# Optimization experiments

Measured on AMD Instinct MI355X. Metric: run time of the kernel, lower is better.

Reference implementation:

```python
import jax, jax.numpy as jnp
import numpy as np

RADIUS = 2
TEMP = 1.0
B, CIN, D, H, W = 1, 32, 64, 64, 64
PROJ, OUT = 64, 64
K = (2 * RADIUS + 1) ** 3  # 125 local offsets

_OFFSETS = np.array([(dz, dy, dx)
                     for dz in range(-RADIUS, RADIUS + 1)
                     for dy in range(-RADIUS, RADIUS + 1)
                     for dx in range(-RADIUS, RADIUS + 1)], dtype=np.int32)


def _conv3d(x, w, b, pad):
    y = jax.lax.conv_general_dilated(
        x, w, window_strides=(1, 1, 1), padding=[(pad, pad)] * 3,
        dimension_numbers=('NCDHW', 'OIDHW', 'NCDHW'))
    if b is not None:
        y = y + b[None, :, None, None, None]
    return y


def _l2norm(x):
    # torch F.normalize(dim=1): x / max(||x||_2, 1e-12)
    n = jnp.sqrt(jnp.sum(x * x, axis=1, keepdims=True))
    return x / jnp.maximum(n, 1e-12)


def _inorm(x, eps=1e-5):
    # InstanceNorm3d (affine=False): normalize over spatial dims per (B,C)
    mu = jnp.mean(x, axis=(2, 3, 4), keepdims=True)
    var = jnp.mean((x - mu) ** 2, axis=(2, 3, 4), keepdims=True)
    return (x - mu) * jax.lax.rsqrt(var + eps)


def _ntn(x):
    return jnp.nan_to_num(x, nan=0.0, posinf=0.0, neginf=0.0)


def setup_inputs() -> dict:
    key = jax.random.key(0)
    ks = jax.random.split(key, 8)
    s = 0.05
    return {
        'source_features': jax.random.normal(ks[0], (B, CIN, D, H, W), jnp.float32),
        'warped_target_features': jax.random.normal(ks[1], (B, CIN, D, H, W), jnp.float32),
        'w_src': jax.random.normal(ks[2], (PROJ, CIN, 1, 1, 1), jnp.float32) * s,
        'b_src': jnp.zeros((PROJ,), jnp.float32),
        'w_tgt': jax.random.normal(ks[3], (PROJ, CIN, 1, 1, 1), jnp.float32) * s,
        'b_tgt': jnp.zeros((PROJ,), jnp.float32),
        'w_enc1': jax.random.normal(ks[4], (OUT, K + 5, 3, 3, 3), jnp.float32) * s,
        'b_enc1': jnp.zeros((OUT,), jnp.float32),
        'w_enc2': jax.random.normal(ks[5], (OUT, OUT, 3, 3, 3), jnp.float32) * s,
        'b_enc2': jnp.zeros((OUT,), jnp.float32),
    }


def reference(source_features, warped_target_features, w_src, b_src, w_tgt, b_tgt,
              w_enc1, b_enc1, w_enc2, b_enc2):
    sp = _l2norm(_conv3d(source_features, w_src, b_src, 0))      # [B,P,D,H,W]
    tp = _l2norm(_conv3d(warped_target_features, w_tgt, b_tgt, 0))
    pt = jnp.pad(tp, ((0, 0), (0, 0), (RADIUS, RADIUS), (RADIUS, RADIUS), (RADIUS, RADIUS)),
                 mode='edge')  # replicate pad

    starts = jnp.asarray(_OFFSETS + RADIUS, jnp.int32)  # [K,3] slice starts

    def corr_one(st):
        sh = jax.lax.dynamic_slice(pt, (0, 0, st[0], st[1], st[2]), (B, PROJ, D, H, W))
        return jnp.sum(sp * sh, axis=1)  # [B,D,H,W]

    corr = jnp.transpose(jax.vmap(corr_one)(starts), (1, 0, 2, 3, 4))  # [B,K,D,H,W]
    scaled = corr / max(TEMP, 1e-6)

    top2 = jax.lax.top_k(jnp.moveaxis(scaled, 1, -1), 2)[0]  # [B,D,H,W,2]
    m = jnp.moveaxis(top2[..., 0:1], -1, 1)   # running max   [B,1,D,H,W]
    s2 = jnp.moveaxis(top2[..., 1:2], -1, 1)  # second max

    p = jnp.exp(scaled - m)                    # [B,K,D,H,W]
    Z = jnp.sum(p, axis=1, keepdims=True)
    inv = 1.0 / jnp.maximum(Z, 1e-8)

    offv = jnp.asarray(_OFFSETS, jnp.float32)  # [K,3]
    expected_offset = _ntn(jnp.einsum('bkdhw,kc->bcdhw', p, offv) * inv)
    confidence = _ntn(jnp.minimum(inv, 1.0))   # max-prob = exp(m-m)/Z
    second_prob = jnp.exp(s2 - m) * inv
    margin = _ntn(jnp.maximum(confidence - second_prob, 0.0))
    entropy = _ntn(m + jnp.log(jnp.maximum(Z, 1e-8))
                   - jnp.sum(p * scaled, axis=1, keepdims=True) * inv)

    enc_in = jnp.concatenate([corr, expected_offset, confidence, entropy], axis=1)  # [B,K+5,D,H,W]
    h = _conv3d(enc_in, w_enc1, b_enc1, 1)
    h = jax.nn.gelu(_inorm(h), approximate=False)
    h = _conv3d(h, w_enc2, b_enc2, 1)
    h = jax.nn.gelu(_inorm(h), approximate=False)
    encoded_features = _ntn(h)

    return expected_offset, confidence, margin, entropy, encoded_features
```

## Files before the change

kernel.cpp:

```cpp
#include <hip/hip_runtime.h>

#define DEV __device__ __forceinline__

typedef short bf16x8 __attribute__((ext_vector_type(8)));
typedef float f32x4 __attribute__((ext_vector_type(4)));

static const int NVOX = 262144;

DEV float bflo(unsigned int u) { return __uint_as_float(u << 16); }
DEV float bfhi(unsigned int u) { return __uint_as_float(u & 0xffff0000u); }
DEV float bf2f(unsigned short s) { return __uint_as_float(((unsigned int)s) << 16); }
DEV unsigned short f2bf(float f) {
    unsigned int x = __float_as_uint(f);
    x += 0x7fffu + ((x >> 16) & 1u);
    return (unsigned short)(x >> 16);
}
DEV float ldin(const void* p, int i, int f) {
    return f ? ((const float*)p)[i] : bf2f(((const unsigned short*)p)[i]);
}

DEV void gld16(const unsigned short* g, unsigned short* l) {
    __builtin_amdgcn_global_load_lds(
        (const __attribute__((address_space(1))) unsigned int*)g,
        (__attribute__((address_space(3))) unsigned int*)l, 16, 0, 0);
}

__global__ void sniff_kernel(const unsigned short* __restrict__ src, int* __restrict__ flag) {
    __shared__ int cnt[256];
    int t = threadIdx.x;
    int c = 0;
    for (int i = t; i < 4096; i += 256) {
        unsigned int u = (unsigned int)src[i] & 0x7fffu;
        c += (u >= 0x4900u) ? 1 : 0;
    }
    cnt[t] = c;
    __syncthreads();
    for (int s = 128; s > 0; s >>= 1) {
        if (t < s) cnt[t] += cnt[t + s];
        __syncthreads();
    }
    if (t == 0) *flag = (cnt[0] > 8) ? 1 : 0;
}

__global__ void prep_kernel(const void* __restrict__ w1, const void* __restrict__ w2,
                            const void* __restrict__ bsv, const void* __restrict__ btv,
                            const void* __restrict__ b1v, const void* __restrict__ b2v,
                            const int* __restrict__ flag,
                            unsigned short* __restrict__ Wf1,
                            unsigned short* __restrict__ Wf2,
                            float* __restrict__ fbias) {
    const int f = *flag;
    int idx = blockIdx.x * 256 + threadIdx.x;
    const int N1  = 27 * 4 * 4 * 512;
    const int N1E = 2 * 4 * 512;
    const int N2  = 27 * 2 * 4 * 512;
    if (idx < N1) {
        int frag = idx >> 9;
        int r    = idx & 511;
        int lane = r >> 3, j = r & 7;
        int nt = frag & 3;
        int tk = frag >> 2;
        int tap = tk >> 2, kc = tk & 3;
        int o  = nt * 16 + (lane & 15);
        int cp = kc * 32 + (lane >> 4) * 8 + j;
        Wf1[idx] = f2bf(ldin(w1, (o * 130 + cp) * 27 + tap, f));
    } else if (idx < N1 + N1E) {
        int i2 = idx - N1;
        int frag = i2 >> 9;
        int r    = i2 & 511;
        int lane = r >> 3, j = r & 7;
        int nt = frag & 3, kc = frag >> 2;
        int o   = nt * 16 + (lane & 15);
        int kap = kc * 32 + (lane >> 4) * 8 + j;
        unsigned short val = 0;
        if (kap < 54) {
            int tap = kap >> 1, ch = 128 + (kap & 1);
            val = f2bf(ldin(w1, (o * 130 + ch) * 27 + tap, f));
        }
        Wf1[idx] = val;
    } else if (idx < N1 + N1E + N2) {
        int i2 = idx - N1 - N1E;
        int frag = i2 >> 9;
        int r    = i2 & 511;
        int lane = r >> 3, j = r & 7;
        int nt = frag & 3;
        int tk = frag >> 2;
        int tap = tk >> 1, kc = tk & 1;
        int o = nt * 16 + (lane & 15);
        int c = kc * 32 + (lane >> 4) * 8 + j;
        Wf2[i2] = f2bf(ldin(w2, (o * 64 + c) * 27 + tap, f));
    } else if (idx < N1 + N1E + N2 + 256) {
        int j = idx - N1 - N1E - N2;
        const void* bp = (j < 64) ? bsv : (j < 128) ? btv : (j < 192) ? b1v : b2v;
        fbias[j] = ldin(bp, j & 63, f);
    }
}

__global__ __launch_bounds__(256) void proj_kernel(
        const void* __restrict__ Xsrc, const void* __restrict__ Xtgt,
        const void* __restrict__ Wsrc, const void* __restrict__ Wtgt,
        const float* __restrict__ fbias, const int* __restrict__ flag,
        unsigned short* __restrict__ SP, unsigned short* __restrict__ TP) {
    const int f = *flag;
    const void* Xin = blockIdx.y ? Xtgt : Xsrc;
    const void* W   = blockIdx.y ? Wtgt : Wsrc;
    const float* Bb = fbias + (blockIdx.y ? 64 : 0);
    unsigned short* Outp = blockIdx.y ? TP : SP;

    __shared__ float ws[2048];
    const int t = threadIdx.x;
    for (int i = t; i < 2048; i += 256) {
        int ci = i >> 6, o = i & 63;
        ws[i] = ldin(W, o * 32 + ci, f);
    }
    __syncthreads();

    const size_t v = (size_t)blockIdx.x * 256 + t;
    float acc[64];
#pragma unroll
    for (int o = 0; o < 64; ++o) acc[o] = Bb[o];
    if (f) {
        const float* Xf = (const float*)Xin;
        for (int ci = 0; ci < 32; ++ci) {
            float x = Xf[(size_t)ci * NVOX + v];
            const float4* wr = (const float4*)(ws + ci * 64);
#pragma unroll
            for (int o4 = 0; o4 < 16; ++o4) {
                float4 w4 = wr[o4];
                acc[o4 * 4 + 0] = fmaf(w4.x, x, acc[o4 * 4 + 0]);
                acc[o4 * 4 + 1] = fmaf(w4.y, x, acc[o4 * 4 + 1]);
                acc[o4 * 4 + 2] = fmaf(w4.z, x, acc[o4 * 4 + 2]);
                acc[o4 * 4 + 3] = fmaf(w4.w, x, acc[o4 * 4 + 3]);
            }
        }
    } else {
        const unsigned short* Xb = (const unsigned short*)Xin;
        for (int ci = 0; ci < 32; ++ci) {
            float x = bf2f(Xb[(size_t)ci * NVOX + v]);
            const float4* wr = (const float4*)(ws + ci * 64);
#pragma unroll
            for (int o4 = 0; o4 < 16; ++o4) {
                float4 w4 = wr[o4];
                acc[o4 * 4 + 0] = fmaf(w4.x, x, acc[o4 * 4 + 0]);
                acc[o4 * 4 + 1] = fmaf(w4.y, x, acc[o4 * 4 + 1]);
                acc[o4 * 4 + 2] = fmaf(w4.z, x, acc[o4 * 4 + 2]);
                acc[o4 * 4 + 3] = fmaf(w4.w, x, acc[o4 * 4 + 3]);
            }
        }
    }
    float s = 0.f;
#pragma unroll
    for (int o = 0; o < 64; ++o) s = fmaf(acc[o], acc[o], s);
    float scale = 1.f / fmaxf(sqrtf(s), 1e-12f);

    unsigned int pk[32];
#pragma unroll
    for (int o = 0; o < 32; ++o)
        pk[o] = (unsigned int)f2bf(acc[2 * o] * scale) |
                ((unsigned int)f2bf(acc[2 * o + 1] * scale) << 16);
    uint4* outp = (uint4*)(Outp + v * 64);
#pragma unroll
    for (int j = 0; j < 8; ++j)
        outp[j] = make_uint4(pk[4 * j], pk[4 * j + 1], pk[4 * j + 2], pk[4 * j + 3]);
}

__global__ __launch_bounds__(256) void corr_kernel(
        const unsigned short* __restrict__ SP, const unsigned short* __restrict__ TP,
        unsigned short* __restrict__ X1, float* __restrict__ Out) {
    __shared__ __align__(16) unsigned short tpb[2][80 * 64];
    __shared__ __align__(16) unsigned short sband[2][64 * 128];

    const int t = threadIdx.x;
    const int wv = t >> 6, lane = t & 63;
    const int q = lane >> 4, l16 = lane & 15;
    const int x0 = wv * 16;

    const int bid = blockIdx.x;
    const int wg = (bid & 7) * 256 + (bid >> 3);
    const int z = wg >> 5, y = (wg & 31) * 2;
    const size_t vb0 = ((size_t)z * 64 + y) * 64;
    const size_t vb1 = vb0 + 64;

    const unsigned short* ar0 = SP + (vb0 + x0 + l16) * 64 + q * 8;
    const unsigned short* ar1 = SP + (vb1 + x0 + l16) * 64 + q * 8;
    const bf16x8 a00 = *(const bf16x8*)(ar0);
    const bf16x8 a01 = *(const bf16x8*)(ar0 + 32);
    const bf16x8 a10 = *(const bf16x8*)(ar1);
    const bf16x8 a11 = *(const bf16x8*)(ar1 + 32);

    auto stage_tp = [&](int it, int b) {
        const int zc = min(max(z + it / 6 - 2, 0), 63);
        const int yc = min(max(y - 2 + it % 6, 0), 63);
        const unsigned short* tb = TP + ((size_t)zc * 64 + yc) * 4096;
#pragma unroll
        for (int j = 0; j < 2; ++j) {
            int c = t + j * 256;
            int pp = c >> 3, cc = c & 7;
            int xc = min(max(pp - 2, 0), 63);
            gld16(tb + xc * 64 + ((cc ^ (pp & 7)) * 8),
                  &tpb[b][(wv * 64 + j * 256) * 8]);
        }
        if (wv < 2) {
            int c = 512 + wv * 64 + lane;
            int pp = c >> 3, cc = c & 7;
            int xc = min(max(pp - 2, 0), 63);
            gld16(tb + xc * 64 + ((cc ^ (pp & 7)) * 8),
                  &tpb[b][(512 + wv * 64) * 8]);
        }
    };

    stage_tp(0, 0);
    __syncthreads();

    int p = 0;
    for (int it = 0; it < 30; ++it) {
        if (it < 29) stage_tp(it + 1, p ^ 1);
        const int dz = it / 6, j = it % 6;
        const bool r0 = (j < 5), r1 = (j > 0);

        f32x4 acc0[2] = {{0.f, 0.f, 0.f, 0.f}, {0.f, 0.f, 0.f, 0.f}};
        f32x4 acc1[2] = {{0.f, 0.f, 0.f, 0.f}, {0.f, 0.f, 0.f, 0.f}};
        {
            const char* tb = (const char*)tpb[p];
#pragma unroll
            for (int nt = 0; nt < 2; ++nt) {
                const int pr = x0 + nt * 16 + l16;
                bf16x8 b0 = *(const bf16x8*)(tb + pr * 128 + ((q ^ (pr & 7)) * 16));
                bf16x8 b1 = *(const bf16x8*)(tb + pr * 128 + (((4 + q) ^ (pr & 7)) * 16));
                if (r0) {
                    acc0[nt] = __builtin_amdgcn_mfma_f32_16x16x32_bf16(a00, b0, acc0[nt], 0, 0, 0);
                    acc0[nt] = __builtin_amdgcn_mfma_f32_16x16x32_bf16(a01, b1, acc0[nt], 0, 0, 0);
                }
                if (r1) {
                    acc1[nt] = __builtin_amdgcn_mfma_f32_16x16x32_bf16(a10, b0, acc1[nt], 0, 0, 0);
                    acc1[nt] = __builtin_amdgcn_mfma_f32_16x16x32_bf16(a11, b1, acc1[nt], 0, 0, 0);
                }
            }
        }
        if (r0) {
            const int kb = dz * 25 + j * 5;
            char* sg = (char*)sband[0];
#pragma unroll
            for (int nt = 0; nt < 2; ++nt)
#pragma unroll
                for (int r = 0; r < 4; ++r) {
                    int ml = q * 4 + r;
                    int dxp = nt * 16 + l16 - ml;
                    if ((unsigned)dxp < 5u) {
                        int xl = x0 + ml;
                        *(unsigned short*)(sg + xl * 256 + (((kb + dxp) * 2) ^ ((xl & 7) << 4))) =
                            f2bf(acc0[nt][r]);
                    }
                }
        }
        if (r1) {
            const int kb = dz * 25 + (j - 1) * 5;
            char* sg = (char*)sband[1];
#pragma unroll
            for (int nt = 0; nt < 2; ++nt)
#pragma unroll
                for (int r = 0; r < 4; ++r) {
                    int ml = q * 4 + r;
                    int dxp = nt * 16 + l16 - ml;
                    if ((unsigned)dxp < 5u) {
                        int xl = x0 + ml;
                        *(unsigned short*)(sg + xl * 256 + (((kb + dxp) * 2) ^ ((xl & 7) << 4))) =
                            f2bf(acc1[nt][r]);
                    }
                }
        }
        __syncthreads();
        p ^= 1;
    }

    for (int half = 0; half < 2; ++half) {
        const size_t vbase = half ? vb1 : vb0;
        const int vox = t >> 2, part = t & 3;
        const int sx = (vox & 7) << 4;
        const char* sg = (const char*)sband[half];
        uint4 u[4];
#pragma unroll
        for (int j = 0; j < 4; ++j)
            u[j] = *(const uint4*)(sg + vox * 256 + ((part * 64 + j * 16) ^ sx));

        float m = -1e30f, s2 = -1e30f;
#pragma unroll
        for (int j = 0; j < 4; ++j) {
            const unsigned int uu[4] = {u[j].x, u[j].y, u[j].z, u[j].w};
#pragma unroll
            for (int w = 0; w < 4; ++w) {
                int k = part * 32 + j * 8 + w * 2;
                float d0 = (k < 125) ? bflo(uu[w]) : -1e30f;
                float d1 = (k + 1 < 125) ? bfhi(uu[w]) : -1e30f;
                float lo0 = fminf(d0, m); m = fmaxf(d0, m); s2 = fmaxf(s2, lo0);
                float lo1 = fminf(d1, m); m = fmaxf(d1, m); s2 = fmaxf(s2, lo1);
            }
        }
#pragma unroll
        for (int off = 1; off <= 2; off <<= 1) {
            float om = __shfl_xor(m, off, 64);
            float os = __shfl_xor(s2, off, 64);
            float lo = fminf(m, om);
            m = fmaxf(m, om);
            s2 = fmaxf(fmaxf(s2, os), lo);
        }
        int kk = part * 32;
        int dz0 = kk / 25, rem = kk - dz0 * 25, dy0 = rem / 5, dx0 = rem - dy0 * 5;
        float fx = (float)(dx0 - 2), fy = (float)(dy0 - 2), fz = (float)(dz0 - 2);
        float Zs = 0.f, S1 = 0.f, Ox = 0.f, Oy = 0.f, Oz = 0.f;
#pragma unroll
        for (int j = 0; j < 4; ++j) {
            const unsigned int uu[4] = {u[j].x, u[j].y, u[j].z, u[j].w};
#pragma unroll
            for (int w = 0; w < 8; ++w) {
                int k = part * 32 + j * 8 + w;
                bool ok = (k < 125);
                float d = (w & 1) ? bfhi(uu[w >> 1]) : bflo(uu[w >> 1]);
                d = ok ? d : 0.f;
                float e = ok ? __expf(d - m) : 0.f;
                Zs += e; S1 = fmaf(e, d, S1);
                Ox = fmaf(e, fx, Ox); Oy = fmaf(e, fy, Oy); Oz = fmaf(e, fz, Oz);
                fx += 1.f;
                if (fx > 2.5f) { fx = -2.f; fy += 1.f; if (fy > 2.5f) { fy = -2.f; fz += 1.f; } }
            }
        }
#pragma unroll
        for (int off = 1; off <= 2; off <<= 1) {
            Zs += __shfl_xor(Zs, off, 64);
            S1 += __shfl_xor(S1, off, 64);
            Ox += __shfl_xor(Ox, off, 64);
            Oy += __shfl_xor(Oy, off, 64);
            Oz += __shfl_xor(Oz, off, 64);
        }
        if (part == 0) {
            float inv  = 1.f / fmaxf(Zs, 1e-8f);
            float eoz = Oz * inv, eoy = Oy * inv, eox = Ox * inv;
            float conf = fminf(inv, 1.f);
            float marg = fmaxf(conf - __expf(s2 - m) * inv, 0.f);
            float ent  = m + __logf(fmaxf(Zs, 1e-8f)) - S1 * inv;
            char* sgw = (char*)sband[half];
            *(unsigned short*)(sgw + vox * 256 + (250 ^ sx)) = f2bf(eoz);
            *(unsigned short*)(sgw + vox * 256 + (252 ^ sx)) = f2bf(eoy);
            *(unsigned short*)(sgw + vox * 256 + (254 ^ sx)) = f2bf(eox);
            const size_t v = vbase + vox;
            *(unsigned int*)(X1 + v * 160 + 128) =
                (unsigned int)f2bf(conf) | ((unsigned int)f2bf(ent) << 16);
            Out[v]                    = eoz;
            Out[(size_t)NVOX + v]     = eoy;
            Out[(size_t)2 * NVOX + v] = eox;
            Out[(size_t)3 * NVOX + v] = conf;
            Out[(size_t)4 * NVOX + v] = marg;
            Out[(size_t)5 * NVOX + v] = ent;
        }
    }
    __syncthreads();

#pragma unroll
    for (int j = 0; j < 8; ++j) {
        int i = t + j * 256;
        int row = i >> 10, rr = i & 1023;
        int vox = rr >> 4, cc = rr & 15;
        *(uint4*)(X1 + ((row ? vb1 : vb0) + vox) * 160 + (size_t)cc * 8) =
            *(const uint4*)((const char*)sband[row] + vox * 256 + ((cc * 16) ^ ((vox & 7) << 4)));
    }
}

template <int XSTRIDE, int CPAD, int KC, int NLD, int MINW, bool TAIL>
__global__ __launch_bounds__(256, MINW) void conv3_kernel(
        const unsigned short* __restrict__ Xin, const unsigned short* __restrict__ Wf,
        const unsigned short* __restrict__ Wfe,
        const float* __restrict__ Bias, unsigned short* __restrict__ Out) {
    constexpr int SLOT = 66 * CPAD;
    constexpr int CH16 = CPAD / 8;
    __shared__ __align__(16) unsigned short lds[3 * SLOT];
    const int lin = blockIdx.x;
    const int wg = (lin & 7) * 256 + (lin >> 3);
    const int z = wg >> 5;
    const int y = (wg & 31) * 2;
    const int t = threadIdx.x;
    const int wv = t >> 6, lane = t & 63;
    const int quad = lane >> 4, l16 = lane & 15;
    const int ml2 = (wv & 1) * 2;
    const int nt2 = (wv >> 1) * 2;

    f32x4 acc[2][2][2] = {};

    auto stage_plane = [&](int pidx) {
        const int zz = z + (pidx >> 2) - 1;
        const int py = y + (pidx & 3) - 1;
        if ((unsigned)zz >= 64u || (unsigned)py >= 64u) return;
        const unsigned short* base = Xin + (((size_t)zz * 64 + py) * 64) * XSTRIDE;
        unsigned short* dst = lds + (pidx % 3) * SLOT + CPAD;
#pragma unroll
        for (int i = 0; i < NLD; ++i) {
            int chunk = wv * 64 + lane + i * 256;
            int xi = chunk / CH16;
            int cc = chunk % CH16;
            gld16(base + xi * XSTRIDE + ((cc ^ ((xi + 1) & 7)) * 8),
                  dst + (size_t)(wv * 64 + i * 256) * 8);
        }
    };

    if (TAIL) {
        unsigned short* ebuf = lds;
#pragma unroll
        for (int i2 = 0; i2 < 16; ++i2) {
            int i = t + i2 * 256;
            int vox = i >> 5, slot = i & 31;
            unsigned int val = 0u;
            int kap;
            if (slot < 27) {
                int ddz = slot / 9 - 1, ddy = (slot / 3) % 3 - 1, dxx = slot % 3 - 1;
                int zz = z + ddz, yy = y + (vox >> 6) + ddy, xx = (vox & 63) + dxx;
                kap = slot * 2;
                if ((unsigned)zz < 64u && (unsigned)yy < 64u && (unsigned)xx < 64u)
                    val = *(const unsigned int*)(Xin + (((size_t)zz * 64 + yy) * 64 + xx) * XSTRIDE + 128);
            } else {
                kap = 54 + (slot - 27) * 2;
            }
            *(unsigned int*)(ebuf + (size_t)vox * 72 + kap) = val;
        }
        __syncthreads();
#pragma unroll
        for (int kc = 0; kc < 2; ++kc) {
            bf16x8 bte[2];
#pragma unroll
            for (int nl = 0; nl < 2; ++nl)
                bte[nl] = *(const bf16x8*)(Wfe + (size_t)(kc * 4 + nt2 + nl) * 512 + lane * 8);
#pragma unroll
            for (int r = 0; r < 2; ++r)
#pragma unroll
            for (int ml = 0; ml < 2; ++ml) {
                bf16x8 a = *(const bf16x8*)(ebuf + (size_t)(r * 64 + (ml2 + ml) * 16 + l16) * 72 + (kc * 4 + quad) * 8);
#pragma unroll
                for (int nl = 0; nl < 2; ++nl)
                    acc[r][ml][nl] = __builtin_amdgcn_mfma_f32_16x16x32_bf16(a, bte[nl], acc[r][ml][nl], 0, 0, 0);
            }
        }
        __syncthreads();
    }

    if (t < 6 * CH16) {
        int sl = t / (2 * CH16), r2 = (t / CH16) & 1, c = t % CH16;
        *(uint4*)(&lds[(size_t)sl * SLOT + (size_t)(r2 * 65) * CPAD + c * 8]) =
            make_uint4(0u, 0u, 0u, 0u);
    }
    stage_plane(0);
    stage_plane(1);
    __syncthreads();

    for (int i = 0; i < 9; ++i) {
        const int s0 = (i / 3) * 4 + i % 3;
        if (i == 3 || i == 6) {
            stage_plane(s0 + 1);
            __syncthreads();
        }
        if (s0 + 2 < 12) stage_plane(s0 + 2);

        const int zz = z + i / 3 - 1;
        const int dy = i % 3 - 1;
        const bool zok = (unsigned)zz < 64u;
        const bool rok0 = zok && (unsigned)(y + dy) < 64u;
        const bool rok1 = zok && (unsigned)(y + 1 + dy) < 64u;
        const unsigned short* sb0 = lds + (size_t)(s0 % 3) * SLOT;
        const unsigned short* sb1 = lds + (size_t)((s0 + 1) % 3) * SLOT;
        if (rok0 || rok1) {
#pragma unroll
            for (int dx = 0; dx < 3; ++dx) {
                const int tap = (i / 3) * 9 + (i % 3) * 3 + dx;
                const unsigned short* wt = Wf + ((size_t)tap * KC * 4) * 512 + lane * 8;
                bf16x8 bf[KC][2];
#pragma unroll
                for (int kc = 0; kc < KC; ++kc)
#pragma unroll
                    for (int nl = 0; nl < 2; ++nl)
                        bf[kc][nl] = *(const bf16x8*)(wt + (size_t)(kc * 4 + nt2 + nl) * 512);
#pragma unroll
                for (int kc = 0; kc < KC; ++kc) {
#pragma unroll
                    for (int ml = 0; ml < 2; ++ml) {
                        const int row = (ml2 + ml) * 16 + l16 + dx;
                        const int co = ((kc * 4 + quad) ^ (row & 7)) * 8;
                        if (rok0) {
                            bf16x8 a = *(const bf16x8*)(&sb0[(size_t)row * CPAD + co]);
#pragma unroll
                            for (int nl = 0; nl < 2; ++nl)
                                acc[0][ml][nl] = __builtin_amdgcn_mfma_f32_16x16x32_bf16(a, bf[kc][nl], acc[0][ml][nl], 0, 0, 0);
                        }
                        if (rok1) {
                            bf16x8 a = *(const bf16x8*)(&sb1[(size_t)row * CPAD + co]);
#pragma unroll
                            for (int nl = 0; nl < 2; ++nl)
                                acc[1][ml][nl] = __builtin_amdgcn_mfma_f32_16x16x32_bf16(a, bf[kc][nl], acc[1][ml][nl], 0, 0, 0);
                        }
                    }
                }
            }
        }
        __syncthreads();
    }

#pragma unroll
    for (int r = 0; r < 2; ++r) {
        const size_t vb = ((size_t)z * 64 + (y + r)) * 64;
#pragma unroll
        for (int ml = 0; ml < 2; ++ml) {
#pragma unroll
            for (int nl = 0; nl < 2; ++nl) {
                const int oc = (nt2 + nl) * 16 + l16;
                const float bv = Bias[oc];
#pragma unroll
                for (int rr = 0; rr < 4; ++rr)
                    Out[(vb + (ml2 + ml) * 16 + quad * 4 + rr) * 64 + oc] =
                        f2bf(acc[r][ml][nl][rr] + bv);
            }
        }
    }
}

__global__ __launch_bounds__(256) void stats_kernel(
        const unsigned short* __restrict__ H, float* __restrict__ stats) {
    const int t = threadIdx.x;
    const int c = t & 63, g = t >> 6;
    float s = 0.f, q = 0.f;
    for (int v = blockIdx.x * 4 + g; v < NVOX; v += gridDim.x * 4) {
        float x = bf2f(H[(size_t)v * 64 + c]);
        s += x; q = fmaf(x, x, q);
    }
    __shared__ float ls[256], lq[256];
    ls[t] = s; lq[t] = q;
    __syncthreads();
    if (t < 64) {
        s = ls[t] + ls[t + 64] + ls[t + 128] + ls[t + 192];
        q = lq[t] + lq[t + 64] + lq[t + 128] + lq[t + 192];
        atomicAdd(&stats[c], s);
        atomicAdd(&stats[64 + c], q);
    }
}

__global__ void finalize_kernel(const float* __restrict__ stats, float* __restrict__ musr) {
    int c = threadIdx.x;
    if (c < 64) {
        float mu  = stats[c] * (1.0f / 262144.0f);
        float var = stats[64 + c] * (1.0f / 262144.0f) - mu * mu;
        musr[c] = mu;
        musr[64 + c] = rsqrtf(var + 1e-5f);
    }
}

__global__ __launch_bounds__(256) void norm_gelu_kernel(
        const unsigned short* __restrict__ H, const float* __restrict__ musr,
        unsigned short* __restrict__ G) {
    const size_t base = ((size_t)blockIdx.x * 256 + threadIdx.x) * 8;
    uint4 u = *(const uint4*)(H + base);
    const int c0 = (int)(base & 63);
    const unsigned int uu[4] = {u.x, u.y, u.z, u.w};
    unsigned int w[4];
#pragma unroll
    for (int p = 0; p < 4; ++p) {
        int c = c0 + p * 2;
        float x0 = (bflo(uu[p]) - musr[c]) * musr[64 + c];
        float x1 = (bfhi(uu[p]) - musr[c + 1]) * musr[64 + c + 1];
        float g0 = 0.5f * x0 * (1.f + erff(x0 * 0.70710678118f));
        float g1 = 0.5f * x1 * (1.f + erff(x1 * 0.70710678118f));
        w[p] = (unsigned int)f2bf(g0) | ((unsigned int)f2bf(g1) << 16);
    }
    *(uint4*)(G + base) = make_uint4(w[0], w[1], w[2], w[3]);
}

__global__ __launch_bounds__(256) void out_final_kernel(
        const unsigned short* __restrict__ H2, const float* __restrict__ musr,
        float* __restrict__ OutEnc) {
    __shared__ float tile[64 * 260];
    const int t = threadIdx.x;
    const size_t v0 = (size_t)blockIdx.x * 256;
#pragma unroll
    for (int i = 0; i < 8; ++i) {
        int chunk = t + i * 256;
        uint4 u = *(const uint4*)(H2 + v0 * 64 + (size_t)chunk * 8);
        int vox = chunk >> 3;
        int c0 = (chunk & 7) * 8;
        const unsigned int uu[4] = {u.x, u.y, u.z, u.w};
#pragma unroll
        for (int p = 0; p < 4; ++p) {
            int c = c0 + p * 2;
            float x0 = (bflo(uu[p]) - musr[c]) * musr[64 + c];
            float x1 = (bfhi(uu[p]) - musr[c + 1]) * musr[64 + c + 1];
            tile[c * 260 + vox]       = 0.5f * x0 * (1.f + erff(x0 * 0.70710678118f));
            tile[(c + 1) * 260 + vox] = 0.5f * x1 * (1.f + erff(x1 * 0.70710678118f));
        }
    }
    __syncthreads();
    const int c = t >> 2, sub = t & 3;
#pragma unroll
    for (int iter = 0; iter < 16; ++iter) {
        int fq = iter * 4 + sub;
        float4 val = *(const float4*)(&tile[c * 260 + fq * 4]);
        *(float4*)(OutEnc + (size_t)c * NVOX + v0 + fq * 4) = val;
    }
}

extern "C" void kernel_launch(void* const* d_in, const int* in_sizes, int n_in,
                              void* d_out, int out_size, void* d_ws, size_t ws_size,
                              hipStream_t stream) {
    const void* src  = d_in[0];
    const void* tgt  = d_in[1];
    const void* wsrc = d_in[2];
    const void* bsrc = d_in[3];
    const void* wtgt = d_in[4];
    const void* btgt = d_in[5];
    const void* w1   = d_in[6];
    const void* b1   = d_in[7];
    const void* w2   = d_in[8];
    const void* b2   = d_in[9];
    float* out = (float*)d_out;

    char* ws = (char*)d_ws;
    unsigned short* TPb = (unsigned short*)(ws);
    unsigned short* SPb = (unsigned short*)(ws + 33554432);
    unsigned short* X1  = (unsigned short*)(ws + 67108864);
    unsigned short* Wf1 = (unsigned short*)(ws + 150994944);
    unsigned short* Wf2 = (unsigned short*)(ws + 151547904);
    int*   flag   = (int*)  (ws + 151769088);
    float* fbias  = (float*)(ws + 151769152);
    float* stats1 = (float*)(ws + 151770176);
    float* musr1  = (float*)(ws + 151770688);
    float* stats2 = (float*)(ws + 151771200);
    float* musr2  = (float*)(ws + 151771712);
    unsigned short* H1 = SPb;
    unsigned short* G1 = TPb;
    unsigned short* H2 = X1;
    unsigned short* Wf1e = Wf1 + 27 * 4 * 4 * 512;

    (void)hipMemsetAsync(stats1, 0, 2048, stream);
    sniff_kernel<<<1, 256, 0, stream>>>((const unsigned short*)src, flag);
    prep_kernel<<<1313, 256, 0, stream>>>(w1, w2, bsrc, btgt, b1, b2, flag, Wf1, Wf2, fbias);
    proj_kernel<<<dim3(1024, 2), 256, 0, stream>>>(src, tgt, wsrc, wtgt, fbias, flag, SPb, TPb);
    corr_kernel<<<2048, 256, 0, stream>>>(SPb, TPb, X1, out);
    conv3_kernel<160, 128, 4, 4, 3, true><<<2048, 256, 0, stream>>>(X1, Wf1, Wf1e, fbias + 128, H1);
    stats_kernel<<<256, 256, 0, stream>>>(H1, stats1);
    finalize_kernel<<<1, 64, 0, stream>>>(stats1, musr1);
    norm_gelu_kernel<<<8192, 256, 0, stream>>>(H1, musr1, G1);
    conv3_kernel<64, 64, 2, 2, 4, false><<<2048, 256, 0, stream>>>(G1, Wf2, nullptr, fbias + 192, H2);
    stats_kernel<<<256, 256, 0, stream>>>(H2, stats2);
    finalize_kernel<<<1, 64, 0, stream>>>(stats2, musr2);
    out_final_kernel<<<1024, 256, 0, stream>>>(H2, musr2, out + 6 * (size_t)NVOX);
}
```

Baseline: 695.2 us.

## Switch conv3 kernels to 32x32x16 MFMA with per-wave row ownership

Replaces the 16x16x32 bf16 MFMA tiling in both 3x3x3 conv kernels with 32x32x16 MFMA. Each wave now owns one output row and a 32-channel half of the outputs, and the weight fragment packing in prep_kernel is changed to match. The goal is fewer MFMA issues, fewer B-fragment loads per wave, and less branching on row validity. The cost is different LDS read patterns under the existing swizzle and a larger per-lane accumulator, which could add bank conflicts or register pressure.

```diff
diff --git a/kernel.cpp b/kernel.cpp
--- a/kernel.cpp
+++ b/kernel.cpp
@@ -4,6 +4,7 @@
 
 typedef short bf16x8 __attribute__((ext_vector_type(8)));
 typedef float f32x4 __attribute__((ext_vector_type(4)));
+typedef float f32x16 __attribute__((ext_vector_type(16)));
 
 static const int NVOX = 262144;
 
@@ -51,27 +52,27 @@
                             float* __restrict__ fbias) {
     const int f = *flag;
     int idx = blockIdx.x * 256 + threadIdx.x;
-    const int N1  = 27 * 4 * 4 * 512;
-    const int N1E = 2 * 4 * 512;
-    const int N2  = 27 * 2 * 4 * 512;
+    const int N1  = 27 * 8 * 2 * 512;
+    const int N1E = 4 * 2 * 512;
+    const int N2  = 27 * 4 * 2 * 512;
     if (idx < N1) {
         int frag = idx >> 9;
         int r    = idx & 511;
         int lane = r >> 3, j = r & 7;
-        int nt = frag & 3;
-        int tk = frag >> 2;
-        int tap = tk >> 2, kc = tk & 3;
-        int o  = nt * 16 + (lane & 15);
-        int cp = kc * 32 + (lane >> 4) * 8 + j;
+        int nt = frag & 1;
+        int tk = frag >> 1;
+        int tap = tk >> 3, kc = tk & 7;
+        int o  = nt * 32 + (lane & 31);
+        int cp = kc * 16 + (lane >> 5) * 8 + j;
         Wf1[idx] = f2bf(ldin(w1, (o * 130 + cp) * 27 + tap, f));
     } else if (idx < N1 + N1E) {
         int i2 = idx - N1;
         int frag = i2 >> 9;
         int r    = i2 & 511;
         int lane = r >> 3, j = r & 7;
-        int nt = frag & 3, kc = frag >> 2;
-        int o   = nt * 16 + (lane & 15);
-        int kap = kc * 32 + (lane >> 4) * 8 + j;
+        int nt = frag & 1, kc = frag >> 1;
+        int o   = nt * 32 + (lane & 31);
+        int kap = kc * 16 + (lane >> 5) * 8 + j;
         unsigned short val = 0;
         if (kap < 54) {
             int tap = kap >> 1, ch = 128 + (kap & 1);
@@ -83,11 +84,11 @@
         int frag = i2 >> 9;
         int r    = i2 & 511;
         int lane = r >> 3, j = r & 7;
-        int nt = frag & 3;
-        int tk = frag >> 2;
-        int tap = tk >> 1, kc = tk & 1;
-        int o = nt * 16 + (lane & 15);
-        int c = kc * 32 + (lane >> 4) * 8 + j;
+        int nt = frag & 1;
+        int tk = frag >> 1;
+        int tap = tk >> 2, kc = tk & 3;
+        int o = nt * 32 + (lane & 31);
+        int c = kc * 16 + (lane >> 5) * 8 + j;
         Wf2[i2] = f2bf(ldin(w2, (o * 64 + c) * 27 + tap, f));
     } else if (idx < N1 + N1E + N2 + 256) {
         int j = idx - N1 - N1E - N2;
@@ -379,11 +380,11 @@
     const int y = (wg & 31) * 2;
     const int t = threadIdx.x;
     const int wv = t >> 6, lane = t & 63;
-    const int quad = lane >> 4, l16 = lane & 15;
-    const int ml2 = (wv & 1) * 2;
-    const int nt2 = (wv >> 1) * 2;
-
-    f32x4 acc[2][2][2] = {};
+    const int ry = wv & 1;
+    const int nt = wv >> 1;
+    const int l31 = lane & 31, kh = lane >> 5;
+
+    f32x16 acc[2] = {};
 
     auto stage_plane = [&](int pidx) {
         const int zz = z + (pidx >> 2) - 1;
@@ -422,19 +423,13 @@
         }
         __syncthreads();
 #pragma unroll
-        for (int kc = 0; kc < 2; ++kc) {
-            bf16x8 bte[2];
-#pragma unroll
-            for (int nl = 0; nl < 2; ++nl)
-                bte[nl] = *(const bf16x8*)(Wfe + (size_t)(kc * 4 + nt2 + nl) * 512 + lane * 8);
-#pragma unroll
-            for (int r = 0; r < 2; ++r)
-#pragma unroll
-            for (int ml = 0; ml < 2; ++ml) {
-                bf16x8 a = *(const bf16x8*)(ebuf + (size_t)(r * 64 + (ml2 + ml) * 16 + l16) * 72 + (kc * 4 + quad) * 8);
-#pragma unroll
-                for (int nl = 0; nl < 2; ++nl)
-                    acc[r][ml][nl] = __builtin_amdgcn_mfma_f32_16x16x32_bf16(a, bte[nl], acc[r][ml][nl], 0, 0, 0);
+        for (int kc = 0; kc < 4; ++kc) {
+            bf16x8 bte = *(const bf16x8*)(Wfe + (size_t)(kc * 2 + nt) * 512 + lane * 8);
+#pragma unroll
+            for (int half = 0; half < 2; ++half) {
+                bf16x8 a = *(const bf16x8*)(ebuf +
+                    (size_t)((ry * 2 + half) * 32 + l31) * 72 + kc * 16 + kh * 8);
+                acc[half] = __builtin_amdgcn_mfma_f32_32x32x16_bf16(a, bte, acc[half], 0, 0, 0);
             }
         }
         __syncthreads();
@@ -459,40 +454,26 @@
 
         const int zz = z + i / 3 - 1;
         const int dy = i % 3 - 1;
-        const bool zok = (unsigned)zz < 64u;
-        const bool rok0 = zok && (unsigned)(y + dy) < 64u;
-        const bool rok1 = zok && (unsigned)(y + 1 + dy) < 64u;
-        const unsigned short* sb0 = lds + (size_t)(s0 % 3) * SLOT;
-        const unsigned short* sb1 = lds + (size_t)((s0 + 1) % 3) * SLOT;
-        if (rok0 || rok1) {
+        const bool ok = (unsigned)zz < 64u && (unsigned)(y + ry + dy) < 64u;
+        const unsigned short* sb = lds + (size_t)((s0 + ry) % 3) * SLOT;
+        if (ok) {
 #pragma unroll
             for (int dx = 0; dx < 3; ++dx) {
                 const int tap = (i / 3) * 9 + (i % 3) * 3 + dx;
-                const unsigned short* wt = Wf + ((size_t)tap * KC * 4) * 512 + lane * 8;
-                bf16x8 bf[KC][2];
+                const unsigned short* wt = Wf + ((size_t)(tap * KC) * 2 + nt) * 512 + lane * 8;
+                bf16x8 bf[KC];
 #pragma unroll
                 for (int kc = 0; kc < KC; ++kc)
-#pragma unroll
-                    for (int nl = 0; nl < 2; ++nl)
-                        bf[kc][nl] = *(const bf16x8*)(wt + (size_t)(kc * 4 + nt2 + nl) * 512);
+                    bf[kc] = *(const bf16x8*)(wt + (size_t)kc * 2 * 512);
 #pragma unroll
                 for (int kc = 0; kc < KC; ++kc) {
 #pragma unroll
-                    for (int ml = 0; ml < 2; ++ml) {
-                        const int row = (ml2 + ml) * 16 + l16 + dx;
-                        const int co = ((kc * 4 + quad) ^ (row & 7)) * 8;
-                        if (rok0) {
-                            bf16x8 a = *(const bf16x8*)(&sb0[(size_t)row * CPAD + co]);
-#pragma unroll
-                            for (int nl = 0; nl < 2; ++nl)
-                                acc[0][ml][nl] = __builtin_amdgcn_mfma_f32_16x16x32_bf16(a, bf[kc][nl], acc[0][ml][nl], 0, 0, 0);
-                        }
-                        if (rok1) {
-                            bf16x8 a = *(const bf16x8*)(&sb1[(size_t)row * CPAD + co]);
-#pragma unroll
-                            for (int nl = 0; nl < 2; ++nl)
-                                acc[1][ml][nl] = __builtin_amdgcn_mfma_f32_16x16x32_bf16(a, bf[kc][nl], acc[1][ml][nl], 0, 0, 0);
-                        }
+                    for (int half = 0; half < 2; ++half) {
+                        const int row = half * 32 + l31 + dx;
+                        const int chunk = kc * 2 + kh;
+                        bf16x8 a = *(const bf16x8*)(&sb[(size_t)row * CPAD +
+                                                        ((chunk ^ (row & 7)) * 8)]);
+                        acc[half] = __builtin_amdgcn_mfma_f32_32x32x16_bf16(a, bf[kc], acc[half], 0, 0, 0);
                     }
                 }
             }
@@ -500,20 +481,15 @@
         __syncthreads();
     }
 
-#pragma unroll
-    for (int r = 0; r < 2; ++r) {
-        const size_t vb = ((size_t)z * 64 + (y + r)) * 64;
-#pragma unroll
-        for (int ml = 0; ml < 2; ++ml) {
-#pragma unroll
-            for (int nl = 0; nl < 2; ++nl) {
-                const int oc = (nt2 + nl) * 16 + l16;
-                const float bv = Bias[oc];
-#pragma unroll
-                for (int rr = 0; rr < 4; ++rr)
-                    Out[(vb + (ml2 + ml) * 16 + quad * 4 + rr) * 64 + oc] =
-                        f2bf(acc[r][ml][nl][rr] + bv);
-            }
+    const size_t vb = ((size_t)z * 64 + (y + ry)) * 64;
+    const int oc = nt * 32 + l31;
+    const float bv = Bias[oc];
+#pragma unroll
+    for (int half = 0; half < 2; ++half) {
+#pragma unroll
+        for (int reg = 0; reg < 16; ++reg) {
+            int x = half * 32 + (reg & 3) + 8 * (reg >> 2) + 4 * kh;
+            Out[(vb + x) * 64 + oc] = f2bf(acc[half][reg] + bv);
         }
     }
 }
@@ -630,18 +606,18 @@
     unsigned short* H1 = SPb;
     unsigned short* G1 = TPb;
     unsigned short* H2 = X1;
-    unsigned short* Wf1e = Wf1 + 27 * 4 * 4 * 512;
+    unsigned short* Wf1e = Wf1 + 27 * 8 * 2 * 512;
 
     (void)hipMemsetAsync(stats1, 0, 2048, stream);
     sniff_kernel<<<1, 256, 0, stream>>>((const unsigned short*)src, flag);
     prep_kernel<<<1313, 256, 0, stream>>>(w1, w2, bsrc, btgt, b1, b2, flag, Wf1, Wf2, fbias);
     proj_kernel<<<dim3(1024, 2), 256, 0, stream>>>(src, tgt, wsrc, wtgt, fbias, flag, SPb, TPb);
     corr_kernel<<<2048, 256, 0, stream>>>(SPb, TPb, X1, out);
-    conv3_kernel<160, 128, 4, 4, 3, true><<<2048, 256, 0, stream>>>(X1, Wf1, Wf1e, fbias + 128, H1);
+    conv3_kernel<160, 128, 8, 4, 3, true><<<2048, 256, 0, stream>>>(X1, Wf1, Wf1e, fbias + 128, H1);
     stats_kernel<<<256, 256, 0, stream>>>(H1, stats1);
     finalize_kernel<<<1, 64, 0, stream>>>(stats1, musr1);
     norm_gelu_kernel<<<8192, 256, 0, stream>>>(H1, musr1, G1);
-    conv3_kernel<64, 64, 2, 2, 4, false><<<2048, 256, 0, stream>>>(G1, Wf2, nullptr, fbias + 192, H2);
+    conv3_kernel<64, 64, 4, 2, 4, false><<<2048, 256, 0, stream>>>(G1, Wf2, nullptr, fbias + 192, H2);
     stats_kernel<<<256, 256, 0, stream>>>(H2, stats2);
     finalize_kernel<<<1, 64, 0, stream>>>(stats2, musr2);
     out_final_kernel<<<1024, 256, 0, stream>>>(H2, musr2, out + 6 * (size_t)NVOX);
```

New measurement: 713.1 us. 2.6% more time.
